# Kernel tuning notes

Hardware: AMD Instinct MI355X
Metric: run time of the kernel (lower is better)

The kernel has to match this reference:

```python
import jax, jax.numpy as jnp
import numpy as np

H = 8          # num_heads
DM = 128       # dmodel
BN_EPS = 1e-5


def _linear(x, w, b):
    # w stored as [in, out]
    return x @ w + b


def _relu_mha(q, k, v, qw, qb, kw, kb, vw, vb, ow, ob, mask):
    """TemMulHeadAtte: ReLU on projected Q/K/V, masked softmax, ReLU out-proj.
    q,k: [B,N,T,2*DM]; v: [B,N,T,DM]; mask: broadcastable to [B,N,H,T,T] or None."""
    B, N, T, _ = q.shape
    Q = jax.nn.relu(_linear(q, qw, qb)).reshape(B, N, T, H, -1)  # e = 2*DM/H
    K = jax.nn.relu(_linear(k, kw, kb)).reshape(B, N, T, H, -1)
    V = jax.nn.relu(_linear(v, vw, vb)).reshape(B, N, T, H, -1)  # d = DM/H
    scale = 1.0 / np.sqrt(Q.shape[-1]).astype(np.float32)
    scores = jnp.einsum('bnthe,bnshe->bnhts', Q, K)
    if mask is not None:
        scores = jnp.where(mask, -jnp.inf, scores)
    attn = jax.nn.softmax(scale * scores, axis=-1)  # dropout p=0 -> identity
    out = jnp.einsum('bnhts,bnshd->bnthd', attn, V).reshape(B, N, T, -1)
    return jax.nn.relu(_linear(out, ow, ob))


def setup_inputs() -> dict:
    key = jax.random.key(0)
    ks = iter(jax.random.split(key, 32))
    B, N, T = 16, 207, 24
    def w(shape, scale=0.05):
        return (jax.random.normal(next(ks), shape, dtype=jnp.float32) * scale)
    inp = {
        'x': w((B, N, T, DM), 1.0),
        'hidden': w((B, N, T, DM), 1.0),
        'tXin': w((B, N, T, DM), 1.0),
    }
    dk = 2 * DM // H * H   # 256
    dv = DM // H * H       # 128
    for pre in ('s', 't'):  # space / temporal attention params
        inp[pre + 'q_w'] = w((2 * DM, dk)); inp[pre + 'q_b'] = w((dk,))
        inp[pre + 'k_w'] = w((2 * DM, dk)); inp[pre + 'k_b'] = w((dk,))
        inp[pre + 'v_w'] = w((DM, dv));     inp[pre + 'v_b'] = w((dv,))
        inp[pre + 'o_w'] = w((dv, DM));     inp[pre + 'o_b'] = w((DM,))
    inp['gate_w'] = w((2 * DM, DM)); inp['gate_b'] = w((DM,))
    inp['bn_gamma'] = jnp.ones((DM,), jnp.float32)
    inp['bn_beta'] = jnp.zeros((DM,), jnp.float32)
    return inp


def reference(x, hidden, tXin,
              sq_w, sq_b, sk_w, sk_b, sv_w, sv_b, so_w, so_b,
              tq_w, tq_b, tk_w, tk_b, tv_w, tv_b, to_w, to_b,
              gate_w, gate_b, bn_gamma, bn_beta):
    B, N, T, E = hidden.shape
    ht = jnp.concatenate([hidden, tXin], axis=3)  # [B,N,T,2*DM]
    # spatial attention: attend over nodes (N<->T permute)
    sqk = ht.transpose(0, 2, 1, 3)        # [B,T,N,2*DM]
    sval = hidden.transpose(0, 2, 1, 3)   # [B,T,N,DM]
    spaceOut = _relu_mha(sqk, sqk, sval, sq_w, sq_b, sk_w, sk_b, sv_w, sv_b,
                         so_w, so_b, None).transpose(0, 2, 1, 3)  # [B,N,T,DM]
    # temporal attention with causal (strict upper-tri) mask
    mask = jnp.triu(jnp.ones((T, T), dtype=bool), 1)[None, None, None]
    tempOut = _relu_mha(ht, ht, hidden, tq_w, tq_b, tk_w, tk_b, tv_w, tv_b,
                        to_w, to_b, mask)  # [B,N,T,DM]
    # gate + BatchNorm2d over channel dim (training-mode batch stats, biased var)
    gi = _linear(jnp.concatenate([spaceOut, tempOut], axis=3), gate_w, gate_b)
    mean = gi.mean(axis=(0, 1, 2))
    var = gi.var(axis=(0, 1, 2))
    z = jax.nn.sigmoid((gi - mean) * jax.lax.rsqrt(var + BN_EPS) * bn_gamma + bn_beta)
    return z * spaceOut + (1.0 - z) * tempOut
```

## Files before the change

### kernel.cpp

```cpp
#include <hip/hip_runtime.h>
#include <hip/hip_bf16.h>

typedef __bf16 bf16;
typedef __bf16 bf16x8 __attribute__((ext_vector_type(8)));
typedef float f32x4 __attribute__((ext_vector_type(4)));

#define MTOT 79488
#define NDIM 207
#define TDIM 24

#define EXP2F(x) __builtin_amdgcn_exp2f(x)

__global__ void detect_dtype(const void* __restrict__ hidden, int* __restrict__ flag)
{
    __shared__ int cnt;
    if (threadIdx.x == 0) cnt = 0;
    __syncthreads();
    const bf16* h = (const bf16*)hidden;
    int local = 0;
    for (int i = threadIdx.x; i < 4096; i += 256) {
        float v = (float)h[i];
        if (!(fabsf(v) < 1e6f)) local++;
    }
    atomicAdd(&cnt, local);
    __syncthreads();
    if (threadIdx.x == 0) *flag = (cnt > 8) ? 1 : 0;
}

__device__ inline float ld_ext(const void* p, int idx, int isF32)
{
    return isF32 ? ((const float*)p)[idx] : (float)((const bf16*)p)[idx];
}

__global__ __launch_bounds__(256) void cvt_inputs(
    const void* __restrict__ hidden, const void* __restrict__ tXin,
    bf16* __restrict__ hb, bf16* __restrict__ tb, const int* __restrict__ dtf)
{
    const int isF32 = *dtf;
    const void* src = blockIdx.y ? tXin : hidden;
    bf16* dst = blockIdx.y ? tb : hb;
    const size_t e8 = ((size_t)blockIdx.x * 256 + threadIdx.x) * 8;
    bf16x8 v;
    if (isF32) {
        f32x4 lo = *(const f32x4*)((const float*)src + e8);
        f32x4 hi = *(const f32x4*)((const float*)src + e8 + 4);
        v[0]=(bf16)lo[0]; v[1]=(bf16)lo[1]; v[2]=(bf16)lo[2]; v[3]=(bf16)lo[3];
        v[4]=(bf16)hi[0]; v[5]=(bf16)hi[1]; v[6]=(bf16)hi[2]; v[7]=(bf16)hi[3];
    } else {
        v = *(const bf16x8*)((const bf16*)src + e8);
    }
    *(bf16x8*)(dst + e8) = v;
}

__global__ __launch_bounds__(256) void prep_weights(
    const void* __restrict__ sq, const void* __restrict__ sk, const void* __restrict__ sv,
    const void* __restrict__ so, const void* __restrict__ tq, const void* __restrict__ tk,
    const void* __restrict__ tv, const void* __restrict__ to_, const void* __restrict__ gw,
    const void* __restrict__ sqb, const void* __restrict__ skb, const void* __restrict__ svb,
    const void* __restrict__ sob, const void* __restrict__ tqb, const void* __restrict__ tkb,
    const void* __restrict__ tvb, const void* __restrict__ tob, const void* __restrict__ gb,
    bf16* __restrict__ wdst, bf16* __restrict__ bdst, const int* __restrict__ dtf)
{
    const int isF32 = *dtf;
    if (blockIdx.x == 1536) {
        for (int j = threadIdx.x; j < 1664; j += 256) {
            const void* src; int i2;
            if      (j < 256)  { src = sqb; i2 = j; }
            else if (j < 512)  { src = skb; i2 = j - 256; }
            else if (j < 640)  { src = svb; i2 = j - 512; }
            else if (j < 896)  { src = tqb; i2 = j - 640; }
            else if (j < 1152) { src = tkb; i2 = j - 896; }
            else if (j < 1280) { src = tvb; i2 = j - 1152; }
            else if (j < 1408) { src = sob; i2 = j - 1280; }
            else if (j < 1536) { src = tob; i2 = j - 1408; }
            else               { src = gb;  i2 = j - 1536; }
            bdst[j] = (bf16)ld_ext(src, i2, isF32);
        }
        return;
    }
    const int e = blockIdx.x * 256 + threadIdx.x;
    float v;
    if (e < 327680) {
        int br = (e >= 163840);
        int e2 = e - br * 163840;
        int n = e2 >> 8, k = e2 & 255;
        const void* qw = br ? tq : sq;
        const void* kw = br ? tk : sk;
        const void* vw = br ? tv : sv;
        if      (n < 256) v = ld_ext(qw, k * 256 + n, isF32);
        else if (n < 512) v = ld_ext(kw, k * 256 + (n - 256), isF32);
        else              v = (k < 128) ? ld_ext(vw, k * 128 + (n - 512), isF32) : 0.f;
    } else if (e < 360448) {
        int br = (e >= 344064);
        int e2 = e - 327680 - br * 16384;
        int n = e2 >> 7, k = e2 & 127;
        v = ld_ext(br ? to_ : so, k * 128 + n, isF32);
    } else {
        int e2 = e - 360448;
        int n = e2 >> 8, k = e2 & 255;
        v = ld_ext(gw, k * 128 + n, isF32);
    }
    wdst[e] = (bf16)v;
}

__global__ __launch_bounds__(256) void gemm_bt(
    const void* __restrict__ A0v, const void* __restrict__ A1v,
    const bf16* __restrict__ Bt, const bf16* __restrict__ bias,
    bf16* __restrict__ C, int Nout, int Ktot, int doRelu, int aExt,
    const int* __restrict__ dtf, int permMode, float* __restrict__ stats)
{
    const int aF32 = aExt & *dtf;
    __shared__ bf16 As[128 * 72];
    __shared__ bf16 Bs[128 * 72];
    __shared__ float lsum[128], lsq[128];
    const int tid  = threadIdx.x;
    const int wid  = tid >> 6, lane = tid & 63;
    const int wm   = (wid >> 1) * 64, wn = (wid & 1) * 64;
    const int quad = lane >> 4, l16 = lane & 15;
    const int m0   = blockIdx.x * 128, n0 = blockIdx.y * 128;
    const int lrow = tid >> 3;
    const int lcol = (tid & 7) * 8;

    f32x4 acc[4][4] = {};

    for (int k0 = 0; k0 < Ktot; k0 += 64) {
        const void* Ap = (k0 < 128) ? A0v : A1v;
        const int koff = (k0 < 128) ? k0 : k0 - 128;
        #pragma unroll
        for (int p = 0; p < 4; ++p) {
            int r = lrow + p * 32;
            bf16x8 av;
            if (aF32) {
                const float* Af = (const float*)Ap;
                f32x4 lo = *(const f32x4*)(Af + (size_t)(m0 + r) * 128 + koff + lcol);
                f32x4 hi = *(const f32x4*)(Af + (size_t)(m0 + r) * 128 + koff + lcol + 4);
                av[0]=(bf16)lo[0]; av[1]=(bf16)lo[1]; av[2]=(bf16)lo[2]; av[3]=(bf16)lo[3];
                av[4]=(bf16)hi[0]; av[5]=(bf16)hi[1]; av[6]=(bf16)hi[2]; av[7]=(bf16)hi[3];
            } else {
                av = *(const bf16x8*)((const bf16*)Ap + (size_t)(m0 + r) * 128 + koff + lcol);
            }
            *(bf16x8*)&As[r * 72 + lcol] = av;
        }
        #pragma unroll
        for (int p = 0; p < 4; ++p) {
            int r = lrow + p * 32;
            *(bf16x8*)&Bs[r * 72 + lcol] =
                *(const bf16x8*)(Bt + (size_t)(n0 + r) * Ktot + k0 + lcol);
        }
        __syncthreads();
        #pragma unroll
        for (int kk = 0; kk < 64; kk += 32) {
            bf16x8 af[4], bfr[4];
            #pragma unroll
            for (int i = 0; i < 4; ++i)
                af[i] = *(const bf16x8*)&As[(wm + i * 16 + l16) * 72 + kk + quad * 8];
            #pragma unroll
            for (int j = 0; j < 4; ++j)
                bfr[j] = *(const bf16x8*)&Bs[(wn + j * 16 + l16) * 72 + kk + quad * 8];
            #pragma unroll
            for (int i = 0; i < 4; ++i)
                #pragma unroll
                for (int j = 0; j < 4; ++j)
                    acc[i][j] = __builtin_amdgcn_mfma_f32_16x16x32_bf16(
                        af[i], bfr[j], acc[i][j], 0, 0, 0);
        }
        __syncthreads();
    }

    int orow[4][4];
    #pragma unroll
    for (int i = 0; i < 4; ++i)
        #pragma unroll
        for (int r = 0; r < 4; ++r) {
            int m = m0 + wm + i * 16 + quad * 4 + r;
            int o;
            if (permMode == 1) {
                int t = m % 24, bn = m / 24;
                int n = bn % 207, b = bn / 207;
                o = (b * 24 + t) * 207 + n;
            } else if (permMode == 2) {
                int n = m % 207, bt = m / 207;
                int t = bt % 24, b = bt / 24;
                o = (b * 207 + n) * 24 + t;
            } else {
                o = m;
            }
            orow[i][r] = o;
        }

    if (stats) {
        if (tid < 128) { lsum[tid] = 0.f; lsq[tid] = 0.f; }
        __syncthreads();
    }
    #pragma unroll
    for (int j = 0; j < 4; ++j) {
        int col = n0 + wn + j * 16 + l16;
        float bv = (float)bias[col];
        float ps = 0.f, psq = 0.f;
        #pragma unroll
        for (int i = 0; i < 4; ++i) {
            #pragma unroll
            for (int r = 0; r < 4; ++r) {
                float v = acc[i][j][r] + bv;
                if (doRelu) v = fmaxf(v, 0.f);
                if (stats) { ps += v; psq += v * v; }
                C[(size_t)orow[i][r] * Nout + col] = (bf16)v;
            }
        }
        if (stats) {
            atomicAdd(&lsum[col & 127], ps);
            atomicAdd(&lsq[col & 127], psq);
        }
    }
    if (stats) {
        __syncthreads();
        if (tid < 128) {
            atomicAdd(&stats[tid], lsum[tid]);
            atomicAdd(&stats[128 + tid], lsq[tid]);
        }
    }
}

__global__ __launch_bounds__(256) void attn_spatial_mfma(
    const bf16* __restrict__ QKV, bf16* __restrict__ O)
{
    const int hh = blockIdx.x, t = blockIdx.y, b = blockIdx.z;
    __shared__ bf16 Ks[208 * 40];
    __shared__ bf16 Vt[16 * 232];
    __shared__ bf16 Pl[4][2][16 * 40];
    const int tid = threadIdx.x;
    const int wave = tid >> 6, lane = tid & 63;
    const int quad = lane >> 4, l16 = lane & 15;
    const size_t R = (size_t)(b * TDIM + t) * NDIM;

    for (int idx = tid; idx < 832; idx += 256) {
        int n = idx >> 2, seg = (idx & 3) * 8;
        bf16x8 v8 = {};
        if (n < NDIM)
            v8 = *(const bf16x8*)(QKV + (R + n) * 640 + 256 + hh * 32 + seg);
        *(bf16x8*)&Ks[n * 40 + seg] = v8;
    }
    for (int idx = tid; idx < 448; idx += 256) {
        int s = idx >> 1, half = (idx & 1) * 8;
        bf16x8 v8 = {};
        if (s < NDIM)
            v8 = *(const bf16x8*)(QKV + (R + s) * 640 + 512 + hh * 16 + half);
        #pragma unroll
        for (int j = 0; j < 8; ++j)
            Vt[(half + j) * 232 + s] = v8[j];
    }
    __syncthreads();

    const float k2 = 0.25506538410868237f;

    for (int qt = wave; qt < 13; qt += 4) {
        const int q0 = qt * 16;
        int qrow = q0 + l16; if (qrow >= NDIM) qrow = NDIM - 1;
        bf16x8 qfrag = *(const bf16x8*)(QKV + (R + qrow) * 640 + hh * 32 + quad * 8);
        f32x4 s[13];
        #pragma unroll
        for (int c = 0; c < 13; ++c) {
            bf16x8 kf = *(const bf16x8*)&Ks[(c * 16 + l16) * 40 + quad * 8];
            f32x4 z = {};
            s[c] = __builtin_amdgcn_mfma_f32_16x16x32_bf16(qfrag, kf, z, 0, 0, 0);
        }
        float linv[4];
        #pragma unroll
        for (int r = 0; r < 4; ++r) {
            float sum = 0.f;
            #pragma unroll
            for (int c = 0; c < 13; ++c) {
                float p = EXP2F(s[c][r] * k2);
                if (c == 12 && l16 == 15) p = 0.f;
                s[c][r] = p;
                sum += p;
            }
            sum += __shfl_xor(sum, 1);
            sum += __shfl_xor(sum, 2);
            sum += __shfl_xor(sum, 4);
            sum += __shfl_xor(sum, 8);
            linv[r] = __builtin_amdgcn_rcpf(sum);
        }
        f32x4 oacc = {};
        #pragma unroll
        for (int sc = 0; sc < 7; ++sc) {
            bf16* pb = &Pl[wave][sc & 1][0];
            #pragma unroll
            for (int r = 0; r < 4; ++r) {
                float p1 = 0.f;
                if (sc < 6) p1 = s[2 * sc + 1][r];
                pb[(quad * 4 + r) * 40 + l16]      = (bf16)s[2 * sc][r];
                pb[(quad * 4 + r) * 40 + 16 + l16] = (bf16)p1;
            }
            bf16x8 pf = *(const bf16x8*)&pb[l16 * 40 + quad * 8];
            bf16x8 vf = *(const bf16x8*)&Vt[l16 * 232 + sc * 32 + quad * 8];
            oacc = __builtin_amdgcn_mfma_f32_16x16x32_bf16(pf, vf, oacc, 0, 0, 0);
        }
        #pragma unroll
        for (int r = 0; r < 4; ++r) {
            int row = q0 + quad * 4 + r;
            if (row < NDIM)
                O[(R + row) * 128 + hh * 16 + l16] = (bf16)(oacc[r] * linv[r]);
        }
    }
}

__global__ __launch_bounds__(256) void attn_temporal_mfma(
    const bf16* __restrict__ QKV, bf16* __restrict__ O)
{
    const size_t m0 = (size_t)blockIdx.x * TDIM;
    __shared__ bf16 Khs[8 * 32 * 40];
    __shared__ bf16 Vts[8 * 16 * 40];
    __shared__ bf16 Pl[4][2][16 * 40];
    const int tid = threadIdx.x;
    const int wave = tid >> 6, lane = tid & 63;
    const int quad = lane >> 4, l16 = lane & 15;
    const int STR = 640;

    for (int idx = tid; idx < 32 * 32; idx += 256) {
        int row = idx >> 5, seg = idx & 31;
        int h = seg >> 2, j = (seg & 3) * 8;
        bf16x8 v8 = {};
        if (row < TDIM)
            v8 = *(const bf16x8*)(QKV + (m0 + row) * STR + 256 + h * 32 + j);
        *(bf16x8*)&Khs[h * 1280 + row * 40 + j] = v8;
    }
    for (int idx = tid; idx < 32 * 128; idx += 256) {
        int s = idx >> 7, c = idx & 127;
        int h = c >> 4, d = c & 15;
        bf16 v = (bf16)0.f;
        if (s < TDIM) v = QKV[(m0 + s) * STR + 512 + h * 16 + d];
        Vts[h * 640 + d * 40 + s] = v;
    }
    __syncthreads();

    const float k2 = 0.25506538410868237f;

    #pragma unroll
    for (int hi = 0; hi < 2; ++hi) {
        const int h = wave * 2 + hi;
        #pragma unroll
        for (int qt = 0; qt < 2; ++qt) {
            int qrow = qt * 16 + l16; if (qrow >= TDIM) qrow = TDIM - 1;
            bf16x8 qfrag = *(const bf16x8*)(QKV + (m0 + qrow) * STR + h * 32 + quad * 8);
            bf16x8 kf0 = *(const bf16x8*)&Khs[h * 1280 + l16 * 40 + quad * 8];
            bf16x8 kf1 = *(const bf16x8*)&Khs[h * 1280 + (16 + l16) * 40 + quad * 8];
            f32x4 z = {};
            f32x4 s0 = __builtin_amdgcn_mfma_f32_16x16x32_bf16(qfrag, kf0, z, 0, 0, 0);
            f32x4 s1 = __builtin_amdgcn_mfma_f32_16x16x32_bf16(qfrag, kf1, z, 0, 0, 0);
            bf16* pb = &Pl[wave][qt][0];
            float linv[4];
            #pragma unroll
            for (int r = 0; r < 4; ++r) {
                int q = qt * 16 + quad * 4 + r;
                float p0 = (l16 <= q)      ? EXP2F(s0[r] * k2) : 0.f;
                float p1 = (16 + l16 <= q) ? EXP2F(s1[r] * k2) : 0.f;
                float sum = p0 + p1;
                sum += __shfl_xor(sum, 1);
                sum += __shfl_xor(sum, 2);
                sum += __shfl_xor(sum, 4);
                sum += __shfl_xor(sum, 8);
                linv[r] = __builtin_amdgcn_rcpf(sum);
                pb[(quad * 4 + r) * 40 + l16]      = (bf16)p0;
                pb[(quad * 4 + r) * 40 + 16 + l16] = (bf16)p1;
            }
            bf16x8 pf = *(const bf16x8*)&pb[l16 * 40 + quad * 8];
            bf16x8 vf = *(const bf16x8*)&Vts[h * 640 + l16 * 40 + quad * 8];
            f32x4 oacc = __builtin_amdgcn_mfma_f32_16x16x32_bf16(pf, vf, z, 0, 0, 0);
            #pragma unroll
            for (int r = 0; r < 4; ++r) {
                int row = qt * 16 + quad * 4 + r;
                if (row < TDIM)
                    O[(m0 + row) * 128 + h * 16 + l16] = (bf16)(oacc[r] * linv[r]);
            }
        }
    }
}

__global__ __launch_bounds__(256) void bn_final(
    const bf16* __restrict__ gi, const bf16* __restrict__ sp, const bf16* __restrict__ tp,
    const void* __restrict__ gammav, const void* __restrict__ betav,
    const float* __restrict__ stats, void* __restrict__ outv,
    const int* __restrict__ dtf)
{
    const int isF32 = *dtf;
    const size_t base = ((size_t)blockIdx.x * 256 + threadIdx.x) * 8;
    const int c0 = (int)(base & 127);
    const float invM = 1.f / (float)MTOT;
    bf16x8 g8 = *(const bf16x8*)(gi + base);
    bf16x8 s8 = *(const bf16x8*)(sp + base);
    bf16x8 t8 = *(const bf16x8*)(tp + base);
    float res[8];
    #pragma unroll
    for (int j = 0; j < 8; ++j) {
        int c = c0 + j;
        float mean = stats[c] * invM;
        float var  = stats[128 + c] * invM - mean * mean;
        float gam = ld_ext(gammav, c, isF32);
        float bet = ld_ext(betav, c, isF32);
        float g = (float)g8[j];
        float zn = (g - mean) * rsqrtf(var + 1e-5f) * gam + bet;
        float z = 1.f / (1.f + EXP2F(zn * -1.4426950408889634f));
        float sv = (float)s8[j], tv = (float)t8[j];
        res[j] = z * sv + (1.f - z) * tv;
    }
    if (isF32) {
        float* op = (float*)outv + base;
        f32x4 lo = {res[0], res[1], res[2], res[3]};
        f32x4 hi = {res[4], res[5], res[6], res[7]};
        *(f32x4*)op = lo;
        *(f32x4*)(op + 4) = hi;
    } else {
        bf16x8 o8;
        #pragma unroll
        for (int j = 0; j < 8; ++j) o8[j] = (bf16)res[j];
        *(bf16x8*)((bf16*)outv + base) = o8;
    }
}

extern "C" void kernel_launch(void* const* d_in, const int* in_sizes, int n_in,
                              void* d_out, int out_size, void* d_ws, size_t ws_size,
                              hipStream_t stream)
{
    const void* hidden = d_in[1];
    const void* tXin   = d_in[2];
    const void* sq_w = d_in[3];  const void* sq_b = d_in[4];
    const void* sk_w = d_in[5];  const void* sk_b = d_in[6];
    const void* sv_w = d_in[7];  const void* sv_b = d_in[8];
    const void* so_w = d_in[9];  const void* so_b = d_in[10];
    const void* tq_w = d_in[11]; const void* tq_b = d_in[12];
    const void* tk_w = d_in[13]; const void* tk_b = d_in[14];
    const void* tv_w = d_in[15]; const void* tv_b = d_in[16];
    const void* to_w = d_in[17]; const void* to_b = d_in[18];
    const void* gate_w = d_in[19]; const void* gate_b = d_in[20];
    const void* gamma  = d_in[21]; const void* beta   = d_in[22];

    char* ws = (char*)d_ws;
    float* stats = (float*)ws;
    int*  dtf    = (int*)(ws + 1024);
    bf16* bB     = (bf16*)(ws + 2048);
    bf16* wT     = (bf16*)(ws + 8192);
    bf16* spaceO = (bf16*)(ws + 794624);
    bf16* attnO  = (bf16*)(ws + 21143552);
    bf16* QKV    = (bf16*)(ws + 41492480);
    bf16* hb     = (bf16*)(ws + 143237120);
    bf16* tb     = (bf16*)(ws + 163586048);
    bf16* tempO  = attnO;
    bf16* gi     = QKV;

    const int wsBig = (ws_size >= 184000000ull);

    bf16* sW  = wT;            bf16* tW  = wT + 163840;
    bf16* soT = wT + 327680;   bf16* toT = wT + 344064;
    bf16* gwT = wT + 360448;

    (void)hipMemsetAsync(stats, 0, 1024, stream);
    detect_dtype<<<1, 256, 0, stream>>>(hidden, dtf);
    prep_weights<<<dim3(1537), 256, 0, stream>>>(
        sq_w, sk_w, sv_w, so_w, tq_w, tk_w, tv_w, to_w, gate_w,
        sq_b, sk_b, sv_b, so_b, tq_b, tk_b, tv_b, to_b, gate_b,
        wT, bB, dtf);
    if (wsBig)
        cvt_inputs<<<dim3(4968, 2), 256, 0, stream>>>(hidden, tXin, hb, tb, dtf);

    const void* A0 = wsBig ? (const void*)hb : hidden;
    const void* A1 = wsBig ? (const void*)tb : tXin;
    const int aExt = wsBig ? 0 : 1;

    gemm_bt<<<dim3(621, 5), 256, 0, stream>>>(A0, A1, sW, bB, QKV, 640, 256, 1, aExt, dtf, 1, nullptr);
    attn_spatial_mfma<<<dim3(8, TDIM, 16), 256, 0, stream>>>(QKV, attnO);
    gemm_bt<<<dim3(621, 1), 256, 0, stream>>>(attnO, nullptr, soT, bB + 1280, spaceO, 128, 128, 1, 0, dtf, 2, nullptr);

    gemm_bt<<<dim3(621, 5), 256, 0, stream>>>(A0, A1, tW, bB + 640, QKV, 640, 256, 1, aExt, dtf, 0, nullptr);
    attn_temporal_mfma<<<dim3(16 * NDIM), 256, 0, stream>>>(QKV, attnO);
    gemm_bt<<<dim3(621, 1), 256, 0, stream>>>(attnO, nullptr, toT, bB + 1408, tempO, 128, 128, 1, 0, dtf, 0, nullptr);

    gemm_bt<<<dim3(621, 1), 256, 0, stream>>>(spaceO, tempO, gwT, bB + 1536, gi, 128, 256, 0, 0, dtf, 0, stats);
    bn_final<<<dim3(4968), 256, 0, stream>>>(gi, spaceO, tempO, gamma, beta, stats, d_out, dtf);
}
```

Before: 563.9 us.

## Prefetch next K-tile into registers and remap GEMM blocks across XCDs

The GEMM kernel now loads the next K-slice of A and B into registers right after the barrier, so global loads overlap the MFMA work on the current LDS tile instead of stalling before it. The 2D grid is flattened to 1D, and block IDs are remapped so that consecutive logical tiles (the N-tiles that share an M row of A) land on the same XCD, improving L2 reuse of A. The cost is higher register pressure from the prefetch buffers, which may lower occupancy.

```diff
diff --git a/kernel.cpp b/kernel.cpp
--- a/kernel.cpp
+++ b/kernel.cpp
@@ -107,7 +107,7 @@
     const void* __restrict__ A0v, const void* __restrict__ A1v,
     const bf16* __restrict__ Bt, const bf16* __restrict__ bias,
     bf16* __restrict__ C, int Nout, int Ktot, int doRelu, int aExt,
-    const int* __restrict__ dtf, int permMode, float* __restrict__ stats)
+    const int* __restrict__ dtf, int permMode, float* __restrict__ stats, int ntx)
 {
     const int aF32 = aExt & *dtf;
     __shared__ bf16 As[128 * 72];
@@ -117,37 +117,55 @@
     const int wid  = tid >> 6, lane = tid & 63;
     const int wm   = (wid >> 1) * 64, wn = (wid & 1) * 64;
     const int quad = lane >> 4, l16 = lane & 15;
-    const int m0   = blockIdx.x * 128, n0 = blockIdx.y * 128;
+
+    int m0, n0;
+    {
+        const int nwg = (int)gridDim.x;
+        const int lid = (int)blockIdx.x;
+        const int q = nwg >> 3, r = nwg & 7;
+        const int xcd = lid & 7, idx = lid >> 3;
+        const int nid = (xcd < r ? xcd * (q + 1) : r * (q + 1) + (xcd - r) * q) + idx;
+        m0 = (nid / ntx) * 128;
+        n0 = (nid % ntx) * 128;
+    }
+
     const int lrow = tid >> 3;
     const int lcol = (tid & 7) * 8;
 
-    f32x4 acc[4][4] = {};
-
-    for (int k0 = 0; k0 < Ktot; k0 += 64) {
+    bf16x8 av[4], bv[4];
+    auto loadTiles = [&](int k0) {
         const void* Ap = (k0 < 128) ? A0v : A1v;
         const int koff = (k0 < 128) ? k0 : k0 - 128;
         #pragma unroll
         for (int p = 0; p < 4; ++p) {
             int r = lrow + p * 32;
-            bf16x8 av;
             if (aF32) {
                 const float* Af = (const float*)Ap;
                 f32x4 lo = *(const f32x4*)(Af + (size_t)(m0 + r) * 128 + koff + lcol);
                 f32x4 hi = *(const f32x4*)(Af + (size_t)(m0 + r) * 128 + koff + lcol + 4);
-                av[0]=(bf16)lo[0]; av[1]=(bf16)lo[1]; av[2]=(bf16)lo[2]; av[3]=(bf16)lo[3];
-                av[4]=(bf16)hi[0]; av[5]=(bf16)hi[1]; av[6]=(bf16)hi[2]; av[7]=(bf16)hi[3];
+                bf16x8 t;
+                t[0]=(bf16)lo[0]; t[1]=(bf16)lo[1]; t[2]=(bf16)lo[2]; t[3]=(bf16)lo[3];
+                t[4]=(bf16)hi[0]; t[5]=(bf16)hi[1]; t[6]=(bf16)hi[2]; t[7]=(bf16)hi[3];
+                av[p] = t;
             } else {
-                av = *(const bf16x8*)((const bf16*)Ap + (size_t)(m0 + r) * 128 + koff + lcol);
-            }
-            *(bf16x8*)&As[r * 72 + lcol] = av;
-        }
+                av[p] = *(const bf16x8*)((const bf16*)Ap + (size_t)(m0 + r) * 128 + koff + lcol);
+            }
+            bv[p] = *(const bf16x8*)(Bt + (size_t)(n0 + r) * Ktot + k0 + lcol);
+        }
+    };
+
+    loadTiles(0);
+    f32x4 acc[4][4] = {};
+
+    for (int k0 = 0; k0 < Ktot; k0 += 64) {
         #pragma unroll
         for (int p = 0; p < 4; ++p) {
             int r = lrow + p * 32;
-            *(bf16x8*)&Bs[r * 72 + lcol] =
-                *(const bf16x8*)(Bt + (size_t)(n0 + r) * Ktot + k0 + lcol);
+            *(bf16x8*)&As[r * 72 + lcol] = av[p];
+            *(bf16x8*)&Bs[r * 72 + lcol] = bv[p];
         }
         __syncthreads();
+        if (k0 + 64 < Ktot) loadTiles(k0 + 64);
         #pragma unroll
         for (int kk = 0; kk < 64; kk += 32) {
             bf16x8 af[4], bfr[4];
@@ -195,13 +213,13 @@
     #pragma unroll
     for (int j = 0; j < 4; ++j) {
         int col = n0 + wn + j * 16 + l16;
-        float bv = (float)bias[col];
+        float bv2 = (float)bias[col];
         float ps = 0.f, psq = 0.f;
         #pragma unroll
         for (int i = 0; i < 4; ++i) {
             #pragma unroll
             for (int r = 0; r < 4; ++r) {
-                float v = acc[i][j][r] + bv;
+                float v = acc[i][j][r] + bv2;
                 if (doRelu) v = fmaxf(v, 0.f);
                 if (stats) { ps += v; psq += v * v; }
                 C[(size_t)orow[i][r] * Nout + col] = (bf16)v;
@@ -467,14 +485,14 @@
     const void* A1 = wsBig ? (const void*)tb : tXin;
     const int aExt = wsBig ? 0 : 1;
 
-    gemm_bt<<<dim3(621, 5), 256, 0, stream>>>(A0, A1, sW, bB, QKV, 640, 256, 1, aExt, dtf, 1, nullptr);
+    gemm_bt<<<dim3(3105), 256, 0, stream>>>(A0, A1, sW, bB, QKV, 640, 256, 1, aExt, dtf, 1, nullptr, 5);
     attn_spatial_mfma<<<dim3(8, TDIM, 16), 256, 0, stream>>>(QKV, attnO);
-    gemm_bt<<<dim3(621, 1), 256, 0, stream>>>(attnO, nullptr, soT, bB + 1280, spaceO, 128, 128, 1, 0, dtf, 2, nullptr);
-
-    gemm_bt<<<dim3(621, 5), 256, 0, stream>>>(A0, A1, tW, bB + 640, QKV, 640, 256, 1, aExt, dtf, 0, nullptr);
+    gemm_bt<<<dim3(621), 256, 0, stream>>>(attnO, nullptr, soT, bB + 1280, spaceO, 128, 128, 1, 0, dtf, 2, nullptr, 1);
+
+    gemm_bt<<<dim3(3105), 256, 0, stream>>>(A0, A1, tW, bB + 640, QKV, 640, 256, 1, aExt, dtf, 0, nullptr, 5);
     attn_temporal_mfma<<<dim3(16 * NDIM), 256, 0, stream>>>(QKV, attnO);
-    gemm_bt<<<dim3(621, 1), 256, 0, stream>>>(attnO, nullptr, toT, bB + 1408, tempO, 128, 128, 1, 0, dtf, 0, nullptr);
-
-    gemm_bt<<<dim3(621, 1), 256, 0, stream>>>(spaceO, tempO, gwT, bB + 1536, gi, 128, 256, 0, 0, dtf, 0, stats);
+    gemm_bt<<<dim3(621), 256, 0, stream>>>(attnO, nullptr, toT, bB + 1408, tempO, 128, 128, 1, 0, dtf, 0, nullptr, 1);
+
+    gemm_bt<<<dim3(621), 256, 0, stream>>>(spaceO, tempO, gwT, bB + 1536, gi, 128, 256, 0, 0, dtf, 0, stats, 1);
     bn_final<<<dim3(4968), 256, 0, stream>>>(gi, spaceO, tempO, gamma, beta, stats, d_out, dtf);
 }
```

Result: faster. 505.7 us (-10.3%).
